# Kernel optimization log

Measured on AMD Instinct MI355X. Metric: run time of the kernel, lower is better.

The kernel has to match this reference:

```python
import jax, jax.numpy as jnp
import numpy as np

R = 2                                   # NMS radius (init kwarg r)
EPS = float(np.finfo(np.float32).eps)   # torch.finfo(float32).eps
PI = float(np.pi)


def _sobel(x):
    """Kornia SpatialGradient (sobel, normalized): x [N,1,H,W] -> (dx, dy) each [N,1,H,W]."""
    kx = jnp.array([[-1., 0., 1.], [-2., 0., 2.], [-1., 0., 1.]], jnp.float32) / 8.0
    ky = kx.T
    k = jnp.stack([kx, ky])[:, None]    # [2,1,3,3] -> out channels dx, dy
    xp = jnp.pad(x, ((0, 0), (0, 0), (1, 1), (1, 1)), mode='edge')  # replicate pad
    out = jax.lax.conv_general_dilated(xp, k, (1, 1), 'VALID',
                                       dimension_numbers=('NCHW', 'OIHW', 'NCHW'))
    return out[:, 0:1], out[:, 1:2]


def _theta(mask):
    """Edge direction from one-hot mask, per STEAL edges_nms. mask [N,1,H,W]."""
    dx, dy = _sobel(mask)
    gxx, _ = _sobel(dx)
    gxy, gyy = _sobel(dy)
    return jnp.fmod(jnp.arctan(gyy * jnp.sign(-gxy + EPS) / (gxx + EPS)), PI)


def setup_inputs() -> dict:
    key = jax.random.key(0)
    k1, k2 = jax.random.split(key)
    pred_labels = jax.random.normal(k1, (4, 16, 512, 1024), dtype=jnp.float32)
    true_labels = jax.random.randint(k2, (4, 512, 1024), 0, 16, dtype=jnp.int64)
    return {"pred_labels": pred_labels, "true_labels": true_labels}


def reference(pred_labels, true_labels):
    B, C, H, W = pred_labels.shape
    # per-class one-hot masks -> direction maps
    onehot = jax.nn.one_hot(true_labels, C, dtype=jnp.float32)        # [B,H,W,C]
    masks = onehot.transpose(0, 3, 1, 2).reshape(B * C, 1, H, W)
    theta = _theta(masks).reshape(B, C, H, W)
    thresh_theta = jnp.fmod(jnp.round(theta * (5.0 / PI)) + 5.0, 5.0)  # {0..4}
    dirs = jnp.fmod(thresh_theta, 4.0).astype(jnp.int32)               # {0,1,2,3}

    exp_p = jnp.exp(pred_labels)
    js = list(range(-R, R))
    # offsets (dx_off, dy_off) summed in the denominator for each direction
    offs = {
        0: [(0, j) for j in js],        # horizontal: preds[x, y-r:y+r]
        1: [(j, -j - 1) for j in js],   # anti-diagonal
        2: [(j, 0) for j in js],        # vertical: preds[x-r:x+r, y]
        3: [(-j - 1, j) for j in js],   # anti-diagonal (reversed traversal, same set)
    }
    denom = jnp.ones_like(exp_p)
    for d in range(4):
        dd = exp_p * 0.0
        for ox, oy in offs[d]:
            dd = dd + jnp.roll(exp_p, (-ox, -oy), axis=(2, 3))  # exp_p[x+ox, y+oy]
        denom = jnp.where(dirs == d, dd, denom)

    interior = jnp.zeros((H, W), bool).at[R:H - R, R:W - R].set(True)
    nms = jnp.where(interior, exp_p / denom, 0.0)
    return jnp.sum(nms)
```

## Files before the change

### kernel.cpp

```cpp
#include <hip/hip_runtime.h>


#define Bn 4
#define Cn 16
#define Hn 512
#define Wn 1024
#define TW 128
#define TH 16
#define LW 132
#define LH 20
#define NT 256

#define EPSF 1.1920928955078125e-07f
#define T1C 0.32491969623290623f
#define T2C 1.3763819204711735f

typedef unsigned long long u64;
typedef unsigned int u32;
typedef float f4u __attribute__((ext_vector_type(4), aligned(4)));
typedef int   i4u __attribute__((ext_vector_type(4), aligned(4)));

static __device__ __forceinline__ float fast_rcp(float x) {
#if __has_builtin(__builtin_amdgcn_rcpf)
  return __builtin_amdgcn_rcpf(x);
#else
  return 1.0f / x;
#endif
}

__global__ __launch_bounds__(NT)
void steal_nms_kernel(const float* __restrict__ pred,
                      const int* __restrict__ labels,
                      float* __restrict__ ws)
{
  __shared__ unsigned char labt[LH][LW];
  __shared__ float ext[LH][LW];
  __shared__ float wsum[NT/64];

  const int w0 = blockIdx.x * TW;
  const int h0 = blockIdx.y * TH;
  const int bz = blockIdx.z;
  const int b  = bz >> 4;
  const int c  = bz & 15;
  const int tid = threadIdx.x;

  const float* plane = pred + (size_t)(b*Cn + c) * (size_t)(Hn*Wn);
  const bool interior = (h0 >= 2) && (h0 + TH + 2 <= Hn) &&
                        (w0 >= 2) && (w0 + TW + 2 <= Wn);

  if (interior) {
    const int*   lb = labels + (size_t)(h0-2)*Wn + (w0-2);
    const float* pb = plane  + (size_t)(h0-2)*Wn + (w0-2);
    for (int i = tid; i < LH*33; i += NT) {
      int row = i / 33;
      int c4  = (i - row*33) * 4;
      i4u L = *(const i4u*)(lb + row*Wn + c4);
      u32 v = (u32)L.x | ((u32)L.y << 8) | ((u32)L.z << 16) | ((u32)L.w << 24);
      *(u32*)&labt[row][c4] = v;
      f4u p = *(const f4u*)(pb + row*Wn + c4);
      float4 e;
      e.x = __expf(p.x); e.y = __expf(p.y); e.z = __expf(p.z); e.w = __expf(p.w);
      *(float4*)&ext[row][c4] = e;
    }
  } else {
    for (int i = tid; i < LH * (LW/4); i += NT) {
      int row  = i / (LW/4);
      int col4 = (i - row*(LW/4)) * 4;
      int gh = h0 - 2 + row; gh = min(max(gh, 0), Hn-1);
      const int* lrow = labels + gh * Wn;
      u32 v = 0;
      #pragma unroll
      for (int k = 0; k < 4; ++k) {
        int gw = w0 - 2 + col4 + k; gw = min(max(gw, 0), Wn-1);
        v |= (u32)(lrow[gw] & 0xff) << (8*k);
      }
      *(u32*)&labt[row][col4] = v;
    }
    for (int i = tid; i < LH*(LW/2); i += NT) {
      int row = i / (LW/2);
      int col = (i - row*(LW/2)) * 2;
      int gh = h0 - 2 + row; gh = min(max(gh, 0), Hn-1);
      int ga = w0 - 2 + col;
      int gb = ga + 1;
      ga = min(max(ga, 0), Wn-1);
      gb = min(max(gb, 0), Wn-1);
      const float* prow = plane + gh*Wn;
      float e0 = __expf(prow[ga]);
      float e1 = __expf(prow[gb]);
      *(float2*)&ext[row][col] = make_float2(e0, e1);
    }
  }
  __syncthreads();

  const int lane = tid & 63;
  const int wq   = tid >> 6;
  const int hr0  = wq * 4;

  u64 mm[TH/4 + 4];
  {
    const int byte0 = 2*lane;
    const int j0 = byte0 >> 2;
    const int sh = (byte0 & 3) * 8;
    const u64 crep = 0x0101010101010101ULL * (u32)c;
    const u64 m80  = 0x8080808080808080ULL;
    #pragma unroll
    for (int r = 0; r < TH/4 + 4; ++r) {
      const u32* rowp = (const u32*)&labt[hr0 + r][0];
      u64 lo = rowp[j0];
      u64 hi = rowp[j0 + 1];
      u64 wvr = ((hi << 32) | lo) >> sh;
      u64 x = wvr ^ crep;
      mm[r] = ((m80 - x) & m80) >> 7;
    }
  }

  const int gw0 = w0 + 2*lane;
  const bool wvalid0 = (gw0     >= 2) && (gw0     < Wn-2);
  const bool wvalid1 = (gw0 + 1 >= 2) && (gw0 + 1 < Wn-2);

  float acc = 0.f;

  float exr[4][5];
  const int fb = 2*lane;
  #pragma unroll
  for (int r = 0; r < 3; ++r) {
    float2 p0 = *(const float2*)&ext[hr0 + r][fb];
    float2 p1 = *(const float2*)&ext[hr0 + r][fb + 2];
    exr[r][0] = p0.x; exr[r][1] = p0.y;
    exr[r][2] = p1.x; exr[r][3] = p1.y;
    exr[r][4] = ext[hr0 + r][fb + 4];
  }

  #pragma unroll
  for (int i = 0; i < TH/4; ++i) {
    {
      const int rn = (i + 3) & 3;
      float2 p0 = *(const float2*)&ext[hr0 + i + 3][fb];
      float2 p1 = *(const float2*)&ext[hr0 + i + 3][fb + 2];
      exr[rn][0] = p0.x; exr[rn][1] = p0.y;
      exr[rn][2] = p1.x; exr[rn][3] = p1.y;
      exr[rn][4] = ext[hr0 + i + 3][fb + 4];
    }

    u64 m0 = mm[i], m1 = mm[i+1], m2 = mm[i+2], m3 = mm[i+3], m4 = mm[i+4];
    u64 s13 = m1 + m3;
    u64 A  = m0 + m4 + (s13 << 2) + (m2 << 2) + (m2 << 1);
    u64 Bb = 0x0404040404040404ULL + (m3 << 1) + m4 - m0 - (m1 << 1);
    u64 Cb = 0x0404040404040404ULL + m0 + m4 - (m2 << 1);

    #define BY(x,k) ((int)((u32)((x) >> (8*(k))) & 0xffu))
    int A0=BY(A,0), A1=BY(A,1), A2=BY(A,2), A3=BY(A,3), A4=BY(A,4), A5=BY(A,5);
    int B0=BY(Bb,0), B1=BY(Bb,1), B2=BY(Bb,2), B3=BY(Bb,3), B4=BY(Bb,4), B5=BY(Bb,5);
    int C0=BY(Cb,0), C1=BY(Cb,1), C2=BY(Cb,2), C3=BY(Cb,3), C4=BY(Cb,4), C5=BY(Cb,5);
    #undef BY

    int gxx0 = A0 + A4 - 2*A2;
    int gxx1 = A1 + A5 - 2*A3;
    int gxyS0 = 2*(B3 - B1) + (B4 - B0);
    int gxyS1 = 2*(B4 - B2) + (B5 - B1);
    int gyy0 = C0 + C4 + 4*(C1 + C3) + 6*C2 - 64;
    int gyy1 = C1 + C5 + 4*(C2 + C4) + 6*C3 - 64;

    float den0 = fmaf((float)gxx0, 0.015625f, EPSF);
    float den1 = fmaf((float)gxx1, 0.015625f, EPSF);
    float gy0 = (float)gyy0 * 0.015625f;
    float gy1 = (float)gyy1 * 0.015625f;
    float num0 = (gxyS0 > 0) ? -gy0 : gy0;
    float num1 = (gxyS1 > 0) ? -gy1 : gy1;
    float an0 = fabsf(gy0), an1 = fabsf(gy1);
    float ad0 = fabsf(den0), ad1 = fabsf(den1);
    int rb0 = (int)(an0 >= T1C*ad0) + (int)(an0 >= T2C*ad0);
    int rb1 = (int)(an1 >= T1C*ad1) + (int)(an1 >= T2C*ad1);
    bool ng0 = ((__float_as_int(num0) ^ __float_as_int(den0)) < 0);
    bool ng1 = ((__float_as_int(num1) ^ __float_as_int(den1)) < 0);
    int dir0 = ng0 ? ((rb0 == 2) ? 3 : 0) : rb0;
    int dir1 = ng1 ? ((rb1 == 2) ? 3 : 0) : rb1;

    const float* r0 = exr[(i+0)&3];
    const float* r1 = exr[(i+1)&3];
    const float* r2 = exr[(i+2)&3];
    const float* r3 = exr[(i+3)&3];

    float t12 = r2[1] + r2[2];
    float D0a = t12 + r2[0] + r2[3];
    float D0b = t12 + r2[3] + r2[4];
    float D2a = (r0[2] + r1[2]) + (r2[2] + r3[2]);
    float D2b = (r0[3] + r1[3]) + (r2[3] + r3[3]);
    float Dda = (r0[3] + r1[2]) + (r2[1] + r3[0]);
    float Ddb = (r0[4] + r1[3]) + (r2[2] + r3[1]);

    float dena = (dir0 == 0) ? D0a : ((dir0 == 2) ? D2a : Dda);
    float denb = (dir1 == 0) ? D0b : ((dir1 == 2) ? D2b : Ddb);

    const int gh = h0 + hr0 + i;
    const bool hv = (gh >= 2) && (gh < Hn-2);
    float na = (hv && wvalid0) ? r2[2] : 0.f;
    float nb = (hv && wvalid1) ? r2[3] : 0.f;
    acc += na * fast_rcp(dena);
    acc += nb * fast_rcp(denb);
  }

  #pragma unroll
  for (int off = 32; off > 0; off >>= 1)
    acc += __shfl_down(acc, off);
  if (lane == 0) wsum[wq] = acc;
  __syncthreads();
  if (tid == 0) {
    float s = 0.f;
    #pragma unroll
    for (int q = 0; q < NT/64; ++q) s += wsum[q];
    atomicAdd(&ws[(bz << 2) | (blockIdx.x & 3)], s);
  }
}

__global__ __launch_bounds__(64)
void reduce_ws_kernel(const float* __restrict__ ws, float* __restrict__ out)
{
  const int l = threadIdx.x;
  float s = (ws[l] + ws[l + 64]) + (ws[l + 128] + ws[l + 192]);
  #pragma unroll
  for (int off = 32; off > 0; off >>= 1)
    s += __shfl_down(s, off);
  if (l == 0) *out = s;
}

extern "C" void kernel_launch(void* const* d_in, const int* in_sizes, int n_in,
                              void* d_out, int out_size, void* d_ws, size_t ws_size,
                              hipStream_t stream) {
  (void)in_sizes; (void)n_in; (void)ws_size; (void)out_size;
  const float* pred   = (const float*)d_in[0];
  const int*   labels = (const int*)d_in[1];
  float* out = (float*)d_out;
  float* ws  = (float*)d_ws;

  hipMemsetAsync(ws, 0, 256 * sizeof(float), stream);

  dim3 grid(Wn/TW, Hn/TH, Bn*Cn);
  steal_nms_kernel<<<grid, NT, 0, stream>>>(pred, labels, ws);
  reduce_ws_kernel<<<1, 64, 0, stream>>>(ws, out);
}
```

Baseline: 265.4 us.

## Precompute packed per-class edge directions in a separate pre-pass kernel

Adds a first kernel that reads the labels once per batch and computes the 2-bit NMS direction for all 16 classes, packed into one u32 per pixel. The main kernel then reads these packed directions instead of reloading the labels and redoing the Sobel/direction maths for each class. This removes repeated label loads and integer/float direction arithmetic from the per-class kernel. In exchange it adds a kernel launch and an 8 MB direction buffer that is written and then read back 16 times, and it replaces the float threshold comparisons with integer ratio approximations.

```diff
diff --git a/kernel.cpp b/kernel.cpp
--- a/kernel.cpp
+++ b/kernel.cpp
@@ -5,15 +5,6 @@
 #define Cn 16
 #define Hn 512
 #define Wn 1024
-#define TW 128
-#define TH 16
-#define LW 132
-#define LH 20
-#define NT 256
-
-#define EPSF 1.1920928955078125e-07f
-#define T1C 0.32491969623290623f
-#define T2C 1.3763819204711735f
 
 typedef unsigned long long u64;
 typedef unsigned int u32;
@@ -28,12 +19,118 @@
 #endif
 }
 
+
+#define P1TW 128
+#define P1TH 8
+#define P1LW 132
+#define P1LH 12
+
+__global__ __launch_bounds__(256)
+void dir_kernel(const int* __restrict__ labels, u32* __restrict__ dirs)
+{
+  __shared__ unsigned char labt[P1LH][P1LW];
+
+  const int w0 = blockIdx.x * P1TW;
+  const int h0 = blockIdx.y * P1TH;
+  const int b  = blockIdx.z;
+  const int tid = threadIdx.x;
+
+  const int* lbase = labels + (size_t)b * (Hn*Wn);
+  const bool interior = (h0 >= 2) && (h0 + P1TH + 2 <= Hn) &&
+                        (w0 >= 2) && (w0 + P1TW + 2 <= Wn);
+  if (interior) {
+    const int* lb = lbase + (size_t)(h0-2)*Wn + (w0-2);
+    for (int i = tid; i < P1LH*33; i += 256) {
+      int row = i / 33, c4 = (i - row*33) * 4;
+      i4u L = *(const i4u*)(lb + row*Wn + c4);
+      *(u32*)&labt[row][c4] =
+          (u32)L.x | ((u32)L.y << 8) | ((u32)L.z << 16) | ((u32)L.w << 24);
+    }
+  } else {
+    for (int i = tid; i < P1LH*33; i += 256) {
+      int row = i / 33, c4 = (i - row*33) * 4;
+      int gh = min(max(h0-2+row, 0), Hn-1);
+      const int* lr = lbase + gh*Wn;
+      u32 v = 0;
+      #pragma unroll
+      for (int k = 0; k < 4; ++k) {
+        int gw = min(max(w0-2+c4+k, 0), Wn-1);
+        v |= (u32)(lr[gw] & 0xff) << (8*k);
+      }
+      *(u32*)&labt[row][c4] = v;
+    }
+  }
+  __syncthreads();
+
+  const int tcol = tid & 31;
+  const int trow = tid >> 5;
+
+  u64 W[5];
+  #pragma unroll
+  for (int r = 0; r < 5; ++r) {
+    const u32* lp = (const u32*)&labt[trow + r][0];
+    u64 lo = lp[tcol];
+    u64 hi = lp[tcol + 1];
+    W[r] = lo | (hi << 32);
+  }
+
+  u32 pack[4] = {0u, 0u, 0u, 0u};
+
+  #pragma unroll 1
+  for (int c = 0; c < 16; ++c) {
+    const u64 crep = 0x0101010101010101ULL * (u32)c;
+    u64 m[5];
+    #pragma unroll
+    for (int r = 0; r < 5; ++r) {
+      u64 x = W[r] ^ crep;
+      m[r] = ((0x8080808080808080ULL - x) & 0x8080808080808080ULL) >> 7;
+    }
+    u64 t  = m[1] + m[3];
+    u64 VA = m[0] + m[4] + (t << 2) + (m[2] << 2) + (m[2] << 1);
+    u64 VB = ((m[3] << 1) + m[4] + 0x0303030303030303ULL)
+             - (m[0] + (m[1] << 1));
+    u64 VC = (m[0] + m[4] + 0x0202020202020202ULL) - (m[2] << 1);
+    u64 gxxp = (VA + (VA >> 32) + 0x4040404040404040ULL) - ((VA >> 16) << 1);
+    u64 q1   = (VC >> 8) + (VC >> 24);
+    u64 w16  = VC >> 16;
+    u64 gyyp = (VC + (VC >> 32)) + (q1 << 2) + (w16 << 2) + (w16 << 1);
+    u64 gxyp = (((VB >> 24) << 1) + (VB >> 32) + 0x2020202020202020ULL)
+             - (VB + ((VB >> 8) << 1));
+
+    u32 gxxl = (u32)gxxp, gyyl = (u32)gyyp, gxyl = (u32)gxyp;
+    #pragma unroll
+    for (int k = 0; k < 4; ++k) {
+      int gxx = (int)((gxxl >> (8*k)) & 0xffu) - 64;
+      int gyy = (int)((gyyl >> (8*k)) & 0xffu) - 32;
+      int gxyb = (int)((gxyl >> (8*k)) & 0xffu);
+      int ax = gxx < 0 ? -gxx : gxx;
+      int ay = gyy < 0 ? -gyy : gyy;
+      int t1 = (ay * 100  > ax * 33)   ? 1 : 0;
+      int t2 = (ay * 1000 > ax * 1377) ? 1 : 0;
+      int rb = t1 + t2;
+      bool ng = ((gyy < 0) != (gxyb > 32)) != (gxx < 0);
+      int dir = ng ? ((rb == 2) ? 3 : 0) : rb;
+      pack[k] |= (u32)dir << (2*c);
+    }
+  }
+
+  const int gh = h0 + trow;
+  u32* drow = dirs + ((size_t)b*Hn + gh)*Wn + (w0 + 4*tcol);
+  *(uint4*)drow = make_uint4(pack[0], pack[1], pack[2], pack[3]);
+}
+
+
+#define TW 128
+#define TH 16
+#define LW 132
+#define LH 20
+#define NT 256
+
 __global__ __launch_bounds__(NT)
-void steal_nms_kernel(const float* __restrict__ pred,
-                      const int* __restrict__ labels,
-                      float* __restrict__ ws)
+void nms_sum_kernel(const float* __restrict__ pred,
+                    const u32* __restrict__ dirs,
+                    float* __restrict__ slots)
 {
-  __shared__ unsigned char labt[LH][LW];
   __shared__ float ext[LH][LW];
   __shared__ float wsum[NT/64];
 
@@ -44,79 +141,49 @@
   const int c  = bz & 15;
   const int tid = threadIdx.x;
 
+  const int lane = tid & 63;
+  const int wq   = tid >> 6;
+  const int hr0  = wq * 4;
+  const int gw0  = w0 + 2*lane;
+
+  u64 dp[4];
+  {
+    const u32* dbase = dirs + (size_t)b*Hn*Wn;
+    #pragma unroll
+    for (int i = 0; i < 4; ++i) {
+      int gh = h0 + hr0 + i;
+      dp[i] = *(const u64*)(dbase + (size_t)gh*Wn + gw0);
+    }
+  }
+
   const float* plane = pred + (size_t)(b*Cn + c) * (size_t)(Hn*Wn);
   const bool interior = (h0 >= 2) && (h0 + TH + 2 <= Hn) &&
                         (w0 >= 2) && (w0 + TW + 2 <= Wn);
-
   if (interior) {
-    const int*   lb = labels + (size_t)(h0-2)*Wn + (w0-2);
-    const float* pb = plane  + (size_t)(h0-2)*Wn + (w0-2);
+    const float* pb = plane + (size_t)(h0-2)*Wn + (w0-2);
     for (int i = tid; i < LH*33; i += NT) {
-      int row = i / 33;
-      int c4  = (i - row*33) * 4;
-      i4u L = *(const i4u*)(lb + row*Wn + c4);
-      u32 v = (u32)L.x | ((u32)L.y << 8) | ((u32)L.z << 16) | ((u32)L.w << 24);
-      *(u32*)&labt[row][c4] = v;
+      int row = i / 33, c4 = (i - row*33) * 4;
       f4u p = *(const f4u*)(pb + row*Wn + c4);
       float4 e;
       e.x = __expf(p.x); e.y = __expf(p.y); e.z = __expf(p.z); e.w = __expf(p.w);
       *(float4*)&ext[row][c4] = e;
     }
   } else {
-    for (int i = tid; i < LH * (LW/4); i += NT) {
-      int row  = i / (LW/4);
-      int col4 = (i - row*(LW/4)) * 4;
-      int gh = h0 - 2 + row; gh = min(max(gh, 0), Hn-1);
-      const int* lrow = labels + gh * Wn;
-      u32 v = 0;
-      #pragma unroll
-      for (int k = 0; k < 4; ++k) {
-        int gw = w0 - 2 + col4 + k; gw = min(max(gw, 0), Wn-1);
-        v |= (u32)(lrow[gw] & 0xff) << (8*k);
-      }
-      *(u32*)&labt[row][col4] = v;
-    }
     for (int i = tid; i < LH*(LW/2); i += NT) {
       int row = i / (LW/2);
       int col = (i - row*(LW/2)) * 2;
-      int gh = h0 - 2 + row; gh = min(max(gh, 0), Hn-1);
-      int ga = w0 - 2 + col;
-      int gb = ga + 1;
-      ga = min(max(ga, 0), Wn-1);
-      gb = min(max(gb, 0), Wn-1);
+      int gh = min(max(h0-2+row, 0), Hn-1);
+      int ga = min(max(w0-2+col,   0), Wn-1);
+      int gb = min(max(w0-1+col,   0), Wn-1);
       const float* prow = plane + gh*Wn;
-      float e0 = __expf(prow[ga]);
-      float e1 = __expf(prow[gb]);
-      *(float2*)&ext[row][col] = make_float2(e0, e1);
+      *(float2*)&ext[row][col] = make_float2(__expf(prow[ga]), __expf(prow[gb]));
     }
   }
   __syncthreads();
 
-  const int lane = tid & 63;
-  const int wq   = tid >> 6;
-  const int hr0  = wq * 4;
-
-  u64 mm[TH/4 + 4];
-  {
-    const int byte0 = 2*lane;
-    const int j0 = byte0 >> 2;
-    const int sh = (byte0 & 3) * 8;
-    const u64 crep = 0x0101010101010101ULL * (u32)c;
-    const u64 m80  = 0x8080808080808080ULL;
-    #pragma unroll
-    for (int r = 0; r < TH/4 + 4; ++r) {
-      const u32* rowp = (const u32*)&labt[hr0 + r][0];
-      u64 lo = rowp[j0];
-      u64 hi = rowp[j0 + 1];
-      u64 wvr = ((hi << 32) | lo) >> sh;
-      u64 x = wvr ^ crep;
-      mm[r] = ((m80 - x) & m80) >> 7;
-    }
-  }
-
-  const int gw0 = w0 + 2*lane;
   const bool wvalid0 = (gw0     >= 2) && (gw0     < Wn-2);
   const bool wvalid1 = (gw0 + 1 >= 2) && (gw0 + 1 < Wn-2);
+  const u32 sh = 2u * (u32)c;
 
   float acc = 0.f;
 
@@ -132,7 +199,7 @@
   }
 
   #pragma unroll
-  for (int i = 0; i < TH/4; ++i) {
+  for (int i = 0; i < 4; ++i) {
     {
       const int rn = (i + 3) & 3;
       float2 p0 = *(const float2*)&ext[hr0 + i + 3][fb];
@@ -142,39 +209,8 @@
       exr[rn][4] = ext[hr0 + i + 3][fb + 4];
     }
 
-    u64 m0 = mm[i], m1 = mm[i+1], m2 = mm[i+2], m3 = mm[i+3], m4 = mm[i+4];
-    u64 s13 = m1 + m3;
-    u64 A  = m0 + m4 + (s13 << 2) + (m2 << 2) + (m2 << 1);
-    u64 Bb = 0x0404040404040404ULL + (m3 << 1) + m4 - m0 - (m1 << 1);
-    u64 Cb = 0x0404040404040404ULL + m0 + m4 - (m2 << 1);
-
-    #define BY(x,k) ((int)((u32)((x) >> (8*(k))) & 0xffu))
-    int A0=BY(A,0), A1=BY(A,1), A2=BY(A,2), A3=BY(A,3), A4=BY(A,4), A5=BY(A,5);
-    int B0=BY(Bb,0), B1=BY(Bb,1), B2=BY(Bb,2), B3=BY(Bb,3), B4=BY(Bb,4), B5=BY(Bb,5);
-    int C0=BY(Cb,0), C1=BY(Cb,1), C2=BY(Cb,2), C3=BY(Cb,3), C4=BY(Cb,4), C5=BY(Cb,5);
-    #undef BY
-
-    int gxx0 = A0 + A4 - 2*A2;
-    int gxx1 = A1 + A5 - 2*A3;
-    int gxyS0 = 2*(B3 - B1) + (B4 - B0);
-    int gxyS1 = 2*(B4 - B2) + (B5 - B1);
-    int gyy0 = C0 + C4 + 4*(C1 + C3) + 6*C2 - 64;
-    int gyy1 = C1 + C5 + 4*(C2 + C4) + 6*C3 - 64;
-
-    float den0 = fmaf((float)gxx0, 0.015625f, EPSF);
-    float den1 = fmaf((float)gxx1, 0.015625f, EPSF);
-    float gy0 = (float)gyy0 * 0.015625f;
-    float gy1 = (float)gyy1 * 0.015625f;
-    float num0 = (gxyS0 > 0) ? -gy0 : gy0;
-    float num1 = (gxyS1 > 0) ? -gy1 : gy1;
-    float an0 = fabsf(gy0), an1 = fabsf(gy1);
-    float ad0 = fabsf(den0), ad1 = fabsf(den1);
-    int rb0 = (int)(an0 >= T1C*ad0) + (int)(an0 >= T2C*ad0);
-    int rb1 = (int)(an1 >= T1C*ad1) + (int)(an1 >= T2C*ad1);
-    bool ng0 = ((__float_as_int(num0) ^ __float_as_int(den0)) < 0);
-    bool ng1 = ((__float_as_int(num1) ^ __float_as_int(den1)) < 0);
-    int dir0 = ng0 ? ((rb0 == 2) ? 3 : 0) : rb0;
-    int dir1 = ng1 ? ((rb1 == 2) ? 3 : 0) : rb1;
+    int dir0 = (int)(((u32)dp[i]        >> sh) & 3u);
+    int dir1 = (int)(((u32)(dp[i] >> 32) >> sh) & 3u);
 
     const float* r0 = exr[(i+0)&3];
     const float* r1 = exr[(i+1)&3];
@@ -209,15 +245,15 @@
     float s = 0.f;
     #pragma unroll
     for (int q = 0; q < NT/64; ++q) s += wsum[q];
-    atomicAdd(&ws[(bz << 2) | (blockIdx.x & 3)], s);
+    atomicAdd(&slots[(bz << 2) | (blockIdx.x & 3)], s);
   }
 }
 
 __global__ __launch_bounds__(64)
-void reduce_ws_kernel(const float* __restrict__ ws, float* __restrict__ out)
+void reduce_ws_kernel(const float* __restrict__ slots, float* __restrict__ out)
 {
   const int l = threadIdx.x;
-  float s = (ws[l] + ws[l + 64]) + (ws[l + 128] + ws[l + 192]);
+  float s = (slots[l] + slots[l + 64]) + (slots[l + 128] + slots[l + 192]);
   #pragma unroll
   for (int off = 32; off > 0; off >>= 1)
     s += __shfl_down(s, off);
@@ -231,11 +267,13 @@
   const float* pred   = (const float*)d_in[0];
   const int*   labels = (const int*)d_in[1];
   float* out = (float*)d_out;
-  float* ws  = (float*)d_ws;
-
-  hipMemsetAsync(ws, 0, 256 * sizeof(float), stream);
-
-  dim3 grid(Wn/TW, Hn/TH, Bn*Cn);
-  steal_nms_kernel<<<grid, NT, 0, stream>>>(pred, labels, ws);
-  reduce_ws_kernel<<<1, 64, 0, stream>>>(ws, out);
-}
+
+  u32*   dirs  = (u32*)d_ws;
+  float* slots = (float*)((char*)d_ws + (size_t)Bn*Hn*Wn*sizeof(u32));
+
+  hipMemsetAsync(slots, 0, 256 * sizeof(float), stream);
+
+  dir_kernel<<<dim3(Wn/P1TW, Hn/P1TH, Bn), 256, 0, stream>>>(labels, dirs);
+  nms_sum_kernel<<<dim3(Wn/TW, Hn/TH, Bn*Cn), NT, 0, stream>>>(pred, dirs, slots);
+  reduce_ws_kernel<<<1, 64, 0, stream>>>(slots, out);
+}
```

Measured after the change: 263.5 us. About the same (-0.7%).
